# Performance work log

Hardware: AMD Instinct MI355X
Metric: run time of the kernel (lower is better)

## Reference

```python
import jax, jax.numpy as jnp
import numpy as np

B, N, D, P, V = 8, 256, 300, 128, 50001  # batch, seq len, emb dim, proj dim, vocab(+unk)


def setup_inputs() -> dict:
    key = jax.random.key(0)
    ks = jax.random.split(key, 10)
    s = 1.0 / np.sqrt(D)
    sp = 1.0 / np.sqrt(P)
    emb = jax.random.normal(ks[0], (V, D), jnp.float32)
    emb = emb.at[-1].set(0.0)  # unk row zeroed, matches add_unk
    return {
        "sentence": jax.random.randint(ks[1], (B, N), 0, V),
        "emb": emb,
        "Wl": jax.random.uniform(ks[2], (P, D), jnp.float32, -s, s),
        "bl": jnp.zeros((P,), jnp.float32),
        "Wr": jax.random.uniform(ks[3], (P, D), jnp.float32, -s, s),
        "Wo": jax.random.uniform(ks[4], (1, P), jnp.float32, -sp, sp),
        "bo": jnp.zeros((1,), jnp.float32),
        "Ws1": jax.random.uniform(ks[5], (P, D), jnp.float32, -s, s),
        "bs1": jnp.zeros((P,), jnp.float32),
        "Ws2": jax.random.uniform(ks[6], (1, P), jnp.float32, -sp, sp),
        "bs2": jnp.zeros((1,), jnp.float32),
        "We1": jax.random.uniform(ks[7], (P, D), jnp.float32, -s, s),
        "be1": jnp.zeros((P,), jnp.float32),
        "We2": jax.random.uniform(ks[8], (1, P), jnp.float32, -sp, sp),
        "be2": jnp.zeros((1,), jnp.float32),
    }


def reference(sentence, emb, Wl, bl, Wr, Wo, bo, Ws1, bs1, Ws2, bs2, We1, be1, We2, be2):
    x = emb[sentence]                                   # [B,N,D] embedding lookup
    start = jax.nn.relu(x @ Ws1.T + bs1) @ Ws2.T + bs2  # [B,N,1]
    end = jax.nn.relu(x @ We1.T + be1) @ We2.T + be2    # [B,N,1]
    left = x @ Wl.T + bl                                # [B,N,P]
    right = x @ Wr.T                                    # [B,N,P]
    # proj[b,i,j,p] = left[b,j,p] + right[b,i,p]  (unsqueeze(1) + unsqueeze(2))
    proj = left[:, None, :, :] + right[:, :, None, :]   # [B,N,N,P]
    bigram = jax.nn.relu(proj) @ Wo.T + bo              # [B,N,N,1]
    return (bigram, start, end)
```

## Files before the change

kernel.cpp:

```cpp
#include <hip/hip_runtime.h>
#include <hip/hip_bf16.h>

#define NB 8
#define NN 256
#define DD 300
#define PP 128
#define OFF_S (NB * NN * NN)
#define OFF_E (NB * NN * NN + NB * NN)

typedef unsigned short u16;

__device__ __forceinline__ float bf2f(u16 u) {
    union { unsigned int i; float f; } v;
    v.i = ((unsigned int)u) << 16;
    return v.f;
}
__device__ __forceinline__ u16 f2bf(float f) {
    union { float f; unsigned int i; } v;
    v.f = f;
    unsigned int lsb = (v.i >> 16) & 1u;
    v.i += 0x7fffu + lsb;
    return (u16)(v.i >> 16);
}

template<bool BF>
__device__ __forceinline__ float4 ld4(const void* base, int idx) {
    if (BF) {
        ushort4 e = *(const ushort4*)((const u16*)base + idx);
        return make_float4(bf2f(e.x), bf2f(e.y), bf2f(e.z), bf2f(e.w));
    } else {
        return *(const float4*)((const float*)base + idx);
    }
}
template<bool BF>
__device__ __forceinline__ float ld1(const void* base, int idx) {
    return BF ? bf2f(((const u16*)base)[idx]) : ((const float*)base)[idx];
}
template<bool BF>
__device__ __forceinline__ void st1(void* base, int idx, float v) {
    if (BF) ((u16*)base)[idx] = f2bf(v);
    else    ((float*)base)[idx] = v;
}

extern "C" __global__ void detect_kernel(const unsigned int* __restrict__ embU,
                                         int* __restrict__ flag) {
    int lane = threadIdx.x;
    int cnt = 0;
    for (int i = lane; i < 256; i += 64) {
        unsigned int w = embU[i];
        union { unsigned int u; float f; } v;
        v.u = (w & 0xFFFFu) << 16;
        float a = fabsf(v.f);
        if (a == 0.f || (a >= 0.00390625f && a <= 256.f)) cnt++;
    }
    #pragma unroll
    for (int off = 32; off; off >>= 1) cnt += __shfl_down(cnt, off, 64);
    if (lane == 0) *flag = (cnt >= 128) ? 1 : 0;
}

template<bool BF>
__device__ __forceinline__ void tok_body(
    const int* __restrict__ sent, const void* __restrict__ emb,
    const void* __restrict__ Wl,  const void* __restrict__ bl,
    const void* __restrict__ Wr,
    const void* __restrict__ Ws1, const void* __restrict__ bs1,
    const void* __restrict__ Ws2, const void* __restrict__ bs2,
    const void* __restrict__ We1, const void* __restrict__ be1,
    const void* __restrict__ We2, const void* __restrict__ be2,
    float* __restrict__ leftT, float* __restrict__ rightW,
    void* __restrict__ out,
    float (*sx)[304], float (*redS)[128], float (*redE)[128])
{
    const int tid = threadIdx.x;
    const int t0  = blockIdx.x * 8;

    for (int c = tid; c < 600; c += 256) {
        int t = c / 75;
        int q = c - t * 75;
        int idx = sent[t0 + t];
        float4 f = ld4<BF>(emb, idx * DD + (q << 2));
        *(float4*)&sx[t][q << 2] = f;
    }
    __syncthreads();

    const int p     = tid >> 1;
    const int kh    = tid & 1;
    const int based = kh * 152;
    const int nch   = 38 - kh;

    float accL[8], accR[8], accS[8], accE[8];
    #pragma unroll
    for (int t = 0; t < 8; ++t) { accL[t]=0.f; accR[t]=0.f; accS[t]=0.f; accE[t]=0.f; }

    const int wbase = p * DD + based;

    for (int c = 0; c < nch; ++c) {
        const int d4 = c << 2;
        float4 a = ld4<BF>(Wl,  wbase + d4);
        float4 r = ld4<BF>(Wr,  wbase + d4);
        float4 s = ld4<BF>(Ws1, wbase + d4);
        float4 e = ld4<BF>(We1, wbase + d4);
        #pragma unroll
        for (int t = 0; t < 8; ++t) {
            float4 xv = *(const float4*)&sx[t][based + d4];
            accL[t] = fmaf(xv.x, a.x, accL[t]);
            accL[t] = fmaf(xv.y, a.y, accL[t]);
            accL[t] = fmaf(xv.z, a.z, accL[t]);
            accL[t] = fmaf(xv.w, a.w, accL[t]);
            accR[t] = fmaf(xv.x, r.x, accR[t]);
            accR[t] = fmaf(xv.y, r.y, accR[t]);
            accR[t] = fmaf(xv.z, r.z, accR[t]);
            accR[t] = fmaf(xv.w, r.w, accR[t]);
            accS[t] = fmaf(xv.x, s.x, accS[t]);
            accS[t] = fmaf(xv.y, s.y, accS[t]);
            accS[t] = fmaf(xv.z, s.z, accS[t]);
            accS[t] = fmaf(xv.w, s.w, accS[t]);
            accE[t] = fmaf(xv.x, e.x, accE[t]);
            accE[t] = fmaf(xv.y, e.y, accE[t]);
            accE[t] = fmaf(xv.z, e.z, accE[t]);
            accE[t] = fmaf(xv.w, e.w, accE[t]);
        }
    }

    #pragma unroll
    for (int t = 0; t < 8; ++t) {
        accL[t] += __shfl_xor(accL[t], 1, 64);
        accR[t] += __shfl_xor(accR[t], 1, 64);
        accS[t] += __shfl_xor(accS[t], 1, 64);
        accE[t] += __shfl_xor(accE[t], 1, 64);
    }

    if (kh == 0) {
        float blp  = ld1<BF>(bl,  p);
        float bs1p = ld1<BF>(bs1, p);
        float ws2p = ld1<BF>(Ws2, p);
        #pragma unroll
        for (int t = 0; t < 8; ++t) {
            int tg = t0 + t;
            int bb = tg >> 8;
            int jj = tg & 255;
            leftT[((size_t)bb * PP + p) * NN + jj] = accL[t] + blp;
            rightW[(size_t)tg * PP + p]            = accR[t];
            redS[t][p] = fmaxf(accS[t] + bs1p, 0.f) * ws2p;
        }
    } else {
        float be1p = ld1<BF>(be1, p);
        float we2p = ld1<BF>(We2, p);
        #pragma unroll
        for (int t = 0; t < 8; ++t) {
            redE[t][p] = fmaxf(accE[t] + be1p, 0.f) * we2p;
        }
    }
    __syncthreads();

    const int t = tid >> 5;
    const int l = tid & 31;
    float vs = redS[t][l] + redS[t][l + 32] + redS[t][l + 64] + redS[t][l + 96];
    float ve = redE[t][l] + redE[t][l + 32] + redE[t][l + 64] + redE[t][l + 96];
    #pragma unroll
    for (int off = 16; off; off >>= 1) {
        vs += __shfl_down(vs, off, 32);
        ve += __shfl_down(ve, off, 32);
    }
    if (l == 0) {
        st1<BF>(out, OFF_S + t0 + t, vs + ld1<BF>(bs2, 0));
        st1<BF>(out, OFF_E + t0 + t, ve + ld1<BF>(be2, 0));
    }
}

extern "C" __global__ void __launch_bounds__(256)
tok_kernel(const int* __restrict__ sent, const void* __restrict__ emb,
           const void* __restrict__ Wl,  const void* __restrict__ bl,
           const void* __restrict__ Wr,
           const void* __restrict__ Ws1, const void* __restrict__ bs1,
           const void* __restrict__ Ws2, const void* __restrict__ bs2,
           const void* __restrict__ We1, const void* __restrict__ be1,
           const void* __restrict__ We2, const void* __restrict__ be2,
           float* __restrict__ leftT, float* __restrict__ rightW,
           void* __restrict__ out, const int* __restrict__ flag)
{
    __shared__ float sx[8][304];
    __shared__ float redS[8][128];
    __shared__ float redE[8][128];
    if (*flag) {
        tok_body<true >(sent, emb, Wl, bl, Wr, Ws1, bs1, Ws2, bs2,
                        We1, be1, We2, be2, leftT, rightW, out, sx, redS, redE);
    } else {
        tok_body<false>(sent, emb, Wl, bl, Wr, Ws1, bs1, Ws2, bs2,
                        We1, be1, We2, be2, leftT, rightW, out, sx, redS, redE);
    }
}

extern "C" __global__ void __launch_bounds__(256)
big_kernel(const float* __restrict__ leftT, const float* __restrict__ rightW,
           const void* __restrict__ Wo, const void* __restrict__ bo,
           void* __restrict__ outB, const int* __restrict__ flag)
{
    __shared__ float sR[4][128];
    __shared__ float sWo[128];
    const int  tid = threadIdx.x;
    const int  b   = blockIdx.x >> 6;
    const int  i0  = (blockIdx.x & 63) << 2;
    const bool bf  = (*flag != 0);

    if (tid < 128) sWo[tid] = bf ? bf2f(((const u16*)Wo)[tid])
                                 : ((const float*)Wo)[tid];
    for (int c = tid; c < 512; c += 256) {
        int i = c >> 7, pp = c & 127;
        sR[i][pp] = rightW[((size_t)(b * NN + i0 + i)) * PP + pp];
    }
    __syncthreads();

    const int j = tid;
    const float* lp = leftT + (size_t)b * PP * NN + j;
    float acc0 = 0.f, acc1 = 0.f, acc2 = 0.f, acc3 = 0.f;
    #pragma unroll 8
    for (int pth = 0; pth < 128; ++pth) {
        float lv = lp[pth * NN];
        float wo = sWo[pth];
        acc0 = fmaf(fmaxf(lv + sR[0][pth], 0.f), wo, acc0);
        acc1 = fmaf(fmaxf(lv + sR[1][pth], 0.f), wo, acc1);
        acc2 = fmaf(fmaxf(lv + sR[2][pth], 0.f), wo, acc2);
        acc3 = fmaf(fmaxf(lv + sR[3][pth], 0.f), wo, acc3);
    }
    float bov = bf ? bf2f(((const u16*)bo)[0]) : ((const float*)bo)[0];
    size_t ob = ((size_t)(b * NN + i0)) * NN + j;
    if (bf) {
        u16* o = (u16*)outB;
        o[ob]          = f2bf(acc0 + bov);
        o[ob + NN]     = f2bf(acc1 + bov);
        o[ob + 2 * NN] = f2bf(acc2 + bov);
        o[ob + 3 * NN] = f2bf(acc3 + bov);
    } else {
        float* o = (float*)outB;
        o[ob]          = acc0 + bov;
        o[ob + NN]     = acc1 + bov;
        o[ob + 2 * NN] = acc2 + bov;
        o[ob + 3 * NN] = acc3 + bov;
    }
}

extern "C" void kernel_launch(void* const* d_in, const int* in_sizes, int n_in,
                              void* d_out, int out_size, void* d_ws, size_t ws_size,
                              hipStream_t stream) {
    const int*  sent = (const int*)d_in[0];
    const void* emb  = d_in[1];
    const void* Wl   = d_in[2];
    const void* bl   = d_in[3];
    const void* Wr   = d_in[4];
    const void* Wo   = d_in[5];
    const void* bo   = d_in[6];
    const void* Ws1  = d_in[7];
    const void* bs1  = d_in[8];
    const void* Ws2  = d_in[9];
    const void* bs2  = d_in[10];
    const void* We1  = d_in[11];
    const void* be1  = d_in[12];
    const void* We2  = d_in[13];
    const void* be2  = d_in[14];

    int*   flag   = (int*)d_ws;
    float* leftT  = (float*)((char*)d_ws + 1024);
    float* rightW = leftT + (size_t)NB * PP * NN;

    hipLaunchKernelGGL(detect_kernel, dim3(1), dim3(64), 0, stream,
                       (const unsigned int*)emb, flag);
    hipLaunchKernelGGL(tok_kernel, dim3(256), dim3(256), 0, stream,
                       sent, emb, Wl, bl, Wr, Ws1, bs1, Ws2, bs2,
                       We1, be1, We2, be2, leftT, rightW, d_out, flag);
    hipLaunchKernelGGL(big_kernel, dim3(512), dim3(256), 0, stream,
                       leftT, rightW, Wo, bo, d_out, flag);
}
```

Measured before the change: 169.7 us.

## Pre-transpose projection weights into k-major buffer for coalesced token projection

Adds a prep kernel that packs the four projection weight matrices (Wl, Wr, Ws1, We1) into one transposed k-major fp32 buffer of 512 columns. The token kernel then gives each thread two output columns and walks k with coalesced float2 weight loads, broadcasting transposed embeddings from shared memory. This replaces the per-thread strided row reads and the shared-memory reduction for the start/end heads, which now use a wave shuffle. It costs an extra kernel launch and a transpose of about 600 KB of weights on every call.

After: 163.8 us. 1.04x faster.

```diff
diff --git a/kernel.cpp b/kernel.cpp
--- a/kernel.cpp
+++ b/kernel.cpp
@@ -1,24 +1,25 @@
 #include <hip/hip_runtime.h>
-#include <hip/hip_bf16.h>
 
 #define NB 8
 #define NN 256
 #define DD 300
 #define PP 128
+#define NC 512
 #define OFF_S (NB * NN * NN)
 #define OFF_E (NB * NN * NN + NB * NN)
 
 typedef unsigned short u16;
+typedef unsigned int   u32;
 
 __device__ __forceinline__ float bf2f(u16 u) {
-    union { unsigned int i; float f; } v;
-    v.i = ((unsigned int)u) << 16;
+    union { u32 i; float f; } v;
+    v.i = ((u32)u) << 16;
     return v.f;
 }
 __device__ __forceinline__ u16 f2bf(float f) {
-    union { float f; unsigned int i; } v;
+    union { float f; u32 i; } v;
     v.f = f;
-    unsigned int lsb = (v.i >> 16) & 1u;
+    u32 lsb = (v.i >> 16) & 1u;
     v.i += 0x7fffu + lsb;
     return (u16)(v.i >> 16);
 }
@@ -42,13 +43,13 @@
     else    ((float*)base)[idx] = v;
 }
 
-extern "C" __global__ void detect_kernel(const unsigned int* __restrict__ embU,
+extern "C" __global__ void detect_kernel(const u32* __restrict__ embU,
                                          int* __restrict__ flag) {
     int lane = threadIdx.x;
     int cnt = 0;
     for (int i = lane; i < 256; i += 64) {
-        unsigned int w = embU[i];
-        union { unsigned int u; float f; } v;
+        u32 w = embU[i];
+        union { u32 u; float f; } v;
         v.u = (w & 0xFFFFu) << 16;
         float a = fabsf(v.f);
         if (a == 0.f || (a >= 0.00390625f && a <= 256.f)) cnt++;
@@ -59,135 +60,150 @@
 }
 
 template<bool BF>
+__device__ __forceinline__ void prep_body(
+    const void* __restrict__ Wl, const void* __restrict__ Wr,
+    const void* __restrict__ Ws1, const void* __restrict__ We1,
+    float* __restrict__ WTf, float (*tile)[301])
+{
+    const int tid = threadIdx.x;
+    const int c0  = blockIdx.x * 32;
+
+    for (int e = tid; e < 32 * 75; e += 256) {
+        int r = e / 75;
+        int q = e - r * 75;
+        int c = c0 + r;
+        const void* src = (c < 128) ? Wl : (c < 256) ? Wr
+                        : (c < 384) ? Ws1 : We1;
+        float4 f = ld4<BF>(src, (c & 127) * DD + 4 * q);
+        tile[r][4 * q + 0] = f.x;
+        tile[r][4 * q + 1] = f.y;
+        tile[r][4 * q + 2] = f.z;
+        tile[r][4 * q + 3] = f.w;
+    }
+    __syncthreads();
+    for (int e = tid; e < 300 * 32; e += 256) {
+        int k = e >> 5;
+        int c = e & 31;
+        WTf[(size_t)k * NC + c0 + c] = tile[c][k];
+    }
+}
+
+extern "C" __global__ void __launch_bounds__(256)
+prep_kernel(const void* __restrict__ Wl, const void* __restrict__ Wr,
+            const void* __restrict__ Ws1, const void* __restrict__ We1,
+            float* __restrict__ WTf, const int* __restrict__ flag)
+{
+    __shared__ float tile[32][301];
+    if (*flag) prep_body<true >(Wl, Wr, Ws1, We1, WTf, tile);
+    else       prep_body<false>(Wl, Wr, Ws1, We1, WTf, tile);
+}
+
+template<bool BF>
 __device__ __forceinline__ void tok_body(
     const int* __restrict__ sent, const void* __restrict__ emb,
-    const void* __restrict__ Wl,  const void* __restrict__ bl,
-    const void* __restrict__ Wr,
-    const void* __restrict__ Ws1, const void* __restrict__ bs1,
-    const void* __restrict__ Ws2, const void* __restrict__ bs2,
-    const void* __restrict__ We1, const void* __restrict__ be1,
-    const void* __restrict__ We2, const void* __restrict__ be2,
+    const float* __restrict__ WTf,
+    const void* __restrict__ bl,
+    const void* __restrict__ bs1, const void* __restrict__ Ws2,
+    const void* __restrict__ bs2,
+    const void* __restrict__ be1, const void* __restrict__ We2,
+    const void* __restrict__ be2,
     float* __restrict__ leftT, float* __restrict__ rightW,
-    void* __restrict__ out,
-    float (*sx)[304], float (*redS)[128], float (*redE)[128])
+    void* __restrict__ out, float (*sxT)[8], int* sids)
 {
     const int tid = threadIdx.x;
     const int t0  = blockIdx.x * 8;
 
-    for (int c = tid; c < 600; c += 256) {
-        int t = c / 75;
-        int q = c - t * 75;
-        int idx = sent[t0 + t];
-        float4 f = ld4<BF>(emb, idx * DD + (q << 2));
-        *(float4*)&sx[t][q << 2] = f;
-    }
-    __syncthreads();
-
-    const int p     = tid >> 1;
-    const int kh    = tid & 1;
-    const int based = kh * 152;
-    const int nch   = 38 - kh;
-
-    float accL[8], accR[8], accS[8], accE[8];
+    if (tid < 8) sids[tid] = sent[t0 + tid];
+    __syncthreads();
+
+    for (int e = tid; e < DD * 8; e += 256) {
+        int k = e >> 3, t = e & 7;
+        sxT[k][t] = ld1<BF>(emb, sids[t] * DD + k);
+    }
+    __syncthreads();
+
+    float a0[8], a1[8];
     #pragma unroll
-    for (int t = 0; t < 8; ++t) { accL[t]=0.f; accR[t]=0.f; accS[t]=0.f; accE[t]=0.f; }
-
-    const int wbase = p * DD + based;
-
-    for (int c = 0; c < nch; ++c) {
-        const int d4 = c << 2;
-        float4 a = ld4<BF>(Wl,  wbase + d4);
-        float4 r = ld4<BF>(Wr,  wbase + d4);
-        float4 s = ld4<BF>(Ws1, wbase + d4);
-        float4 e = ld4<BF>(We1, wbase + d4);
+    for (int t = 0; t < 8; ++t) { a0[t] = 0.f; a1[t] = 0.f; }
+
+    const float* wp = WTf + 2 * tid;
+    #pragma unroll 4
+    for (int k = 0; k < DD; ++k) {
+        float2 w  = *(const float2*)(wp + (size_t)k * NC);
+        float4 xa = *(const float4*)&sxT[k][0];
+        float4 xb = *(const float4*)&sxT[k][4];
+        a0[0] = fmaf(xa.x, w.x, a0[0]); a1[0] = fmaf(xa.x, w.y, a1[0]);
+        a0[1] = fmaf(xa.y, w.x, a0[1]); a1[1] = fmaf(xa.y, w.y, a1[1]);
+        a0[2] = fmaf(xa.z, w.x, a0[2]); a1[2] = fmaf(xa.z, w.y, a1[2]);
+        a0[3] = fmaf(xa.w, w.x, a0[3]); a1[3] = fmaf(xa.w, w.y, a1[3]);
+        a0[4] = fmaf(xb.x, w.x, a0[4]); a1[4] = fmaf(xb.x, w.y, a1[4]);
+        a0[5] = fmaf(xb.y, w.x, a0[5]); a1[5] = fmaf(xb.y, w.y, a1[5]);
+        a0[6] = fmaf(xb.z, w.x, a0[6]); a1[6] = fmaf(xb.z, w.y, a1[6]);
+        a0[7] = fmaf(xb.w, w.x, a0[7]); a1[7] = fmaf(xb.w, w.y, a1[7]);
+    }
+
+    const int wv = tid >> 6;
+    const int l  = tid & 63;
+    const int p0 = 2 * l, p1 = p0 + 1;
+
+    if (wv == 0) {
+        float b0 = ld1<BF>(bl, p0), b1 = ld1<BF>(bl, p1);
         #pragma unroll
         for (int t = 0; t < 8; ++t) {
-            float4 xv = *(const float4*)&sx[t][based + d4];
-            accL[t] = fmaf(xv.x, a.x, accL[t]);
-            accL[t] = fmaf(xv.y, a.y, accL[t]);
-            accL[t] = fmaf(xv.z, a.z, accL[t]);
-            accL[t] = fmaf(xv.w, a.w, accL[t]);
-            accR[t] = fmaf(xv.x, r.x, accR[t]);
-            accR[t] = fmaf(xv.y, r.y, accR[t]);
-            accR[t] = fmaf(xv.z, r.z, accR[t]);
-            accR[t] = fmaf(xv.w, r.w, accR[t]);
-            accS[t] = fmaf(xv.x, s.x, accS[t]);
-            accS[t] = fmaf(xv.y, s.y, accS[t]);
-            accS[t] = fmaf(xv.z, s.z, accS[t]);
-            accS[t] = fmaf(xv.w, s.w, accS[t]);
-            accE[t] = fmaf(xv.x, e.x, accE[t]);
-            accE[t] = fmaf(xv.y, e.y, accE[t]);
-            accE[t] = fmaf(xv.z, e.z, accE[t]);
-            accE[t] = fmaf(xv.w, e.w, accE[t]);
-        }
-    }
-
-    #pragma unroll
-    for (int t = 0; t < 8; ++t) {
-        accL[t] += __shfl_xor(accL[t], 1, 64);
-        accR[t] += __shfl_xor(accR[t], 1, 64);
-        accS[t] += __shfl_xor(accS[t], 1, 64);
-        accE[t] += __shfl_xor(accE[t], 1, 64);
-    }
-
-    if (kh == 0) {
-        float blp  = ld1<BF>(bl,  p);
-        float bs1p = ld1<BF>(bs1, p);
-        float ws2p = ld1<BF>(Ws2, p);
+            int tg = t0 + t, bb = tg >> 8, jj = tg & 255;
+            leftT[((size_t)bb * PP + p0) * NN + jj] = a0[t] + b0;
+            leftT[((size_t)bb * PP + p1) * NN + jj] = a1[t] + b1;
+        }
+    } else if (wv == 1) {
         #pragma unroll
         for (int t = 0; t < 8; ++t) {
-            int tg = t0 + t;
-            int bb = tg >> 8;
-            int jj = tg & 255;
-            leftT[((size_t)bb * PP + p) * NN + jj] = accL[t] + blp;
-            rightW[(size_t)tg * PP + p]            = accR[t];
-            redS[t][p] = fmaxf(accS[t] + bs1p, 0.f) * ws2p;
-        }
-    } else {
-        float be1p = ld1<BF>(be1, p);
-        float we2p = ld1<BF>(We2, p);
-        #pragma unroll
-        for (int t = 0; t < 8; ++t) {
-            redE[t][p] = fmaxf(accE[t] + be1p, 0.f) * we2p;
-        }
-    }
-    __syncthreads();
-
-    const int t = tid >> 5;
-    const int l = tid & 31;
-    float vs = redS[t][l] + redS[t][l + 32] + redS[t][l + 64] + redS[t][l + 96];
-    float ve = redE[t][l] + redE[t][l + 32] + redE[t][l + 64] + redE[t][l + 96];
-    #pragma unroll
-    for (int off = 16; off; off >>= 1) {
-        vs += __shfl_down(vs, off, 32);
-        ve += __shfl_down(ve, off, 32);
-    }
-    if (l == 0) {
-        st1<BF>(out, OFF_S + t0 + t, vs + ld1<BF>(bs2, 0));
-        st1<BF>(out, OFF_E + t0 + t, ve + ld1<BF>(be2, 0));
+            rightW[(size_t)(t0 + t) * PP + p0] = a0[t];
+            rightW[(size_t)(t0 + t) * PP + p1] = a1[t];
+        }
+    } else {
+        const void* h1 = (wv == 2) ? bs1 : be1;
+        const void* h2 = (wv == 2) ? Ws2 : We2;
+        const void* h3 = (wv == 2) ? bs2 : be2;
+        float b0 = ld1<BF>(h1, p0), b1 = ld1<BF>(h1, p1);
+        float w0 = ld1<BF>(h2, p0), w1 = ld1<BF>(h2, p1);
+        float v[8];
+        #pragma unroll
+        for (int t = 0; t < 8; ++t)
+            v[t] = fmaxf(a0[t] + b0, 0.f) * w0 + fmaxf(a1[t] + b1, 0.f) * w1;
+        #pragma unroll
+        for (int off = 32; off; off >>= 1) {
+            #pragma unroll
+            for (int t = 0; t < 8; ++t) v[t] += __shfl_down(v[t], off, 64);
+        }
+        if (l == 0) {
+            float b2 = ld1<BF>(h3, 0);
+            int base = (wv == 2) ? OFF_S : OFF_E;
+            #pragma unroll
+            for (int t = 0; t < 8; ++t)
+                st1<BF>(out, base + t0 + t, v[t] + b2);
+        }
     }
 }
 
 extern "C" __global__ void __launch_bounds__(256)
 tok_kernel(const int* __restrict__ sent, const void* __restrict__ emb,
-           const void* __restrict__ Wl,  const void* __restrict__ bl,
-           const void* __restrict__ Wr,
-           const void* __restrict__ Ws1, const void* __restrict__ bs1,
-           const void* __restrict__ Ws2, const void* __restrict__ bs2,
-           const void* __restrict__ We1, const void* __restrict__ be1,
-           const void* __restrict__ We2, const void* __restrict__ be2,
+           const float* __restrict__ WTf,
+           const void* __restrict__ bl,
+           const void* __restrict__ bs1, const void* __restrict__ Ws2,
+           const void* __restrict__ bs2,
+           const void* __restrict__ be1, const void* __restrict__ We2,
+           const void* __restrict__ be2,
            float* __restrict__ leftT, float* __restrict__ rightW,
            void* __restrict__ out, const int* __restrict__ flag)
 {
-    __shared__ float sx[8][304];
-    __shared__ float redS[8][128];
-    __shared__ float redE[8][128];
+    __shared__ __align__(16) float sxT[DD][8];
+    __shared__ int sids[8];
     if (*flag) {
-        tok_body<true >(sent, emb, Wl, bl, Wr, Ws1, bs1, Ws2, bs2,
-                        We1, be1, We2, be2, leftT, rightW, out, sx, redS, redE);
-    } else {
-        tok_body<false>(sent, emb, Wl, bl, Wr, Ws1, bs1, Ws2, bs2,
-                        We1, be1, We2, be2, leftT, rightW, out, sx, redS, redE);
+        tok_body<true >(sent, emb, WTf, bl, bs1, Ws2, bs2, be1, We2, be2,
+                        leftT, rightW, out, sxT, sids);
+    } else {
+        tok_body<false>(sent, emb, WTf, bl, bs1, Ws2, bs2, be1, We2, be2,
+                        leftT, rightW, out, sxT, sids);
     }
 }
 
@@ -262,12 +278,15 @@
     int*   flag   = (int*)d_ws;
     float* leftT  = (float*)((char*)d_ws + 1024);
     float* rightW = leftT + (size_t)NB * PP * NN;
+    float* WTf    = rightW + (size_t)NB * NN * PP;
 
     hipLaunchKernelGGL(detect_kernel, dim3(1), dim3(64), 0, stream,
-                       (const unsigned int*)emb, flag);
+                       (const u32*)emb, flag);
+    hipLaunchKernelGGL(prep_kernel, dim3(16), dim3(256), 0, stream,
+                       Wl, Wr, Ws1, We1, WTf, flag);
     hipLaunchKernelGGL(tok_kernel, dim3(256), dim3(256), 0, stream,
-                       sent, emb, Wl, bl, Wr, Ws1, bs1, Ws2, bs2,
-                       We1, be1, We2, be2, leftT, rightW, d_out, flag);
+                       sent, emb, WTf, bl, bs1, Ws2, bs2, be1, We2, be2,
+                       leftT, rightW, d_out, flag);
     hipLaunchKernelGGL(big_kernel, dim3(512), dim3(256), 0, stream,
                        leftT, rightW, Wo, bo, d_out, flag);
 }
```
